# Kernel tuning notes

Measured on AMD Instinct MI355X. Metric: run time of the kernel, lower is better.

## Reference

```python
import jax, jax.numpy as jnp
import numpy as np

B, T, E, H, L, V = 16, 512, 512, 8, 4, 2048
HS = E // H  # head_size = n_embd // n_head
FF = 4 * E


def _ln(x, g, b):
    m = x.mean(-1, keepdims=True)
    v = ((x - m) ** 2).mean(-1, keepdims=True)
    return (x - m) * jax.lax.rsqrt(v + 1e-5) * g + b


def setup_inputs() -> dict:
    key = jax.random.key(0)
    ks = jax.random.split(key, 16)
    s = jnp.float32(0.02)
    return {
        "idx": jax.random.randint(ks[0], (B, T), 0, V),
        "tok_emb": jax.random.normal(ks[1], (V, E), jnp.float32) * s,
        "pos_emb": jax.random.normal(ks[2], (T, E), jnp.float32) * s,
        "Wq": jax.random.normal(ks[3], (L, E, E), jnp.float32) * s,
        "Wk": jax.random.normal(ks[4], (L, E, E), jnp.float32) * s,
        "Wv": jax.random.normal(ks[5], (L, E, E), jnp.float32) * s,
        "rel": jax.random.normal(ks[6], (L, 2 * T - 1, HS), jnp.float32) * s,
        "Wo": jax.random.normal(ks[7], (L, E, E), jnp.float32) * s,
        "bo": jnp.zeros((L, E), jnp.float32),
        "ln1_g": jnp.ones((L, E), jnp.float32),
        "ln1_b": jnp.zeros((L, E), jnp.float32),
        "W1": jax.random.normal(ks[8], (L, E, FF), jnp.float32) * s,
        "b1": jnp.zeros((L, FF), jnp.float32),
        "W2": jax.random.normal(ks[9], (L, FF, E), jnp.float32) * s,
        "b2": jnp.zeros((L, E), jnp.float32),
        "ln2_g": jnp.ones((L, E), jnp.float32),
        "ln2_b": jnp.zeros((L, E), jnp.float32),
        "lnf_g": jnp.ones((E,), jnp.float32),
        "lnf_b": jnp.zeros((E,), jnp.float32),
        "Wlm": jax.random.normal(ks[10], (E, V), jnp.float32) * s,
        "blm": jnp.zeros((V,), jnp.float32),
    }


def reference(idx, tok_emb, pos_emb, Wq, Wk, Wv, rel, Wo, bo, ln1_g, ln1_b,
              W1, b1, W2, b2, ln2_g, ln2_b, lnf_g, lnf_b, Wlm, blm):
    x = tok_emb[idx] + pos_emb[None, :T]  # (B,T,E)
    ri = jnp.arange(T)
    rel_idx = ri[:, None] - ri[None, :] + (T - 1)  # block_size == T
    causal = ri[:, None] >= ri[None, :]            # (T,T) lower-triangular
    scale = jnp.float32(1.0 / np.sqrt(HS))
    for l in range(L):
        h = _ln(x, ln1_g[l], ln1_b[l])
        # NOTE: torch code does .view(B, H, T, HS) on a (B, T, H*HS) tensor
        # (NOT a transpose) -- jnp.reshape matches row-major view semantics.
        q = (h @ Wq[l]).reshape(B, H, T, HS)
        k = (h @ Wk[l]).reshape(B, H, T, HS)
        v = (h @ Wv[l]).reshape(B, H, T, HS)
        re = rel[l][rel_idx]  # (T,T,HS)
        # rel scores: sum_d q[b,h,i,d]*re[i,j,d]; avoid the 5D intermediate
        scores = jnp.einsum('bhid,bhjd->bhij', q, k) * scale \
               + jnp.einsum('bhid,ijd->bhij', q, re)
        scores = jnp.where(causal, scores, -jnp.inf)
        att = jax.nn.softmax(scores, axis=-1)  # dropout disabled (eval)
        ctx = jnp.einsum('bhij,bhjd->bhid', att, v)
        ctx = jnp.swapaxes(ctx, 1, 2).reshape(B, T, H * HS)
        x = x + ctx @ Wo[l] + bo[l]
        h2 = _ln(x, ln2_g[l], ln2_b[l])
        x = x + jax.nn.relu(h2 @ W1[l] + b1[l]) @ W2[l] + b2[l]
    x = _ln(x, lnf_g, lnf_b)
    return x @ Wlm + blm  # logits (B,T,V)
```

## Files before the change

### kernel.cpp

```cpp
#include <hip/hip_runtime.h>
#include <hip/hip_bf16.h>
#include <stdint.h>

typedef __hip_bfloat16 bf16;
typedef __attribute__((ext_vector_type(8))) short bf16x8;
typedef __attribute__((ext_vector_type(8))) short short8;
typedef __attribute__((ext_vector_type(4))) float f32x4;

#define DEV __device__ __forceinline__

static constexpr int Bn = 16, Tn = 512, En = 512, Hn = 8, Ln = 4, Vn = 2048;
static constexpr int HSn = 64, FFn = 2048, Mn = Bn * Tn;
static constexpr int SQ = 1536;

DEV f32x4 mfma16(bf16x8 a, bf16x8 b, f32x4 c) {
  return __builtin_amdgcn_mfma_f32_16x16x32_bf16(a, b, c, 0, 0, 0);
}
DEV float b2f(bf16 x) { return __bfloat162float(x); }
DEV bf16 f2b(float x) { return __float2bfloat16(x); }
DEV short f2s(float x) { bf16 h = f2b(x); return reinterpret_cast<short&>(h); }

DEV void gload16(const void* g, void* l) {
  __builtin_amdgcn_global_load_lds(
      (const __attribute__((address_space(1))) void*)(uintptr_t)g,
      (__attribute__((address_space(3))) void*)(uint32_t)(uintptr_t)l, 16, 0, 0);
}

__global__ __launch_bounds__(256) void ktranspose(const float* __restrict__ in,
                                                  bf16* __restrict__ out, int R, int C,
                                                  long in_zs, long out_zs) {
  __shared__ float tile[32][33];
  int z = blockIdx.z;
  const float* inz = in + (size_t)z * in_zs;
  bf16* outz = out + (size_t)z * out_zs;
  int c0 = blockIdx.x * 32, r0 = blockIdx.y * 32;
  for (int k = 0; k < 32; k += 8)
    tile[threadIdx.y + k][threadIdx.x] =
        inz[(size_t)(r0 + threadIdx.y + k) * C + (c0 + threadIdx.x)];
  __syncthreads();
  for (int k = 0; k < 32; k += 8)
    outz[(size_t)(c0 + threadIdx.y + k) * R + (r0 + threadIdx.x)] =
        f2b(tile[threadIdx.x][threadIdx.y + k]);
}

__global__ __launch_bounds__(256) void kcast(const float* __restrict__ in,
                                             bf16* __restrict__ out, int n) {
  int i = blockIdx.x * 256 + threadIdx.x;
  if (i < n) out[i] = f2b(in[i]);
}

__global__ __launch_bounds__(256) void kembed(const int* __restrict__ idx,
                                              const float* __restrict__ tok,
                                              const float* __restrict__ pos,
                                              float* __restrict__ x) {
  int i = blockIdx.x * 256 + threadIdx.x;
  int e4 = (i & 127) * 4;
  int bt = i >> 7;
  int t = bt & (Tn - 1);
  f32x4 tv = *(const f32x4*)(tok + (size_t)idx[bt] * En + e4);
  f32x4 pv = *(const f32x4*)(pos + (size_t)t * En + e4);
  *(f32x4*)(x + (size_t)bt * En + e4) = tv + pv;
}

__global__ __launch_bounds__(256) void kln(const float* __restrict__ x,
                                           const float* __restrict__ g,
                                           const float* __restrict__ b,
                                           bf16* __restrict__ out) {
  int row = blockIdx.x * 4 + (threadIdx.x >> 6);
  int lane = threadIdx.x & 63;
  const float* xr = x + (size_t)row * En + lane * 8;
  f32x4 a0 = *(const f32x4*)xr;
  f32x4 a1 = *(const f32x4*)(xr + 4);
  float s = a0[0] + a0[1] + a0[2] + a0[3] + a1[0] + a1[1] + a1[2] + a1[3];
  for (int m = 1; m < 64; m <<= 1) s += __shfl_xor(s, m);
  float mean = s * (1.f / En);
  float s2 = 0.f;
  for (int j = 0; j < 4; j++) { float d0 = a0[j] - mean, d1 = a1[j] - mean; s2 += d0 * d0 + d1 * d1; }
  for (int m = 1; m < 64; m <<= 1) s2 += __shfl_xor(s2, m);
  float rstd = rsqrtf(s2 * (1.f / En) + 1e-5f);
  f32x4 g0 = *(const f32x4*)(g + lane * 8), g1 = *(const f32x4*)(g + lane * 8 + 4);
  f32x4 b0 = *(const f32x4*)(b + lane * 8), b1 = *(const f32x4*)(b + lane * 8 + 4);
  short8 ov;
  for (int j = 0; j < 4; j++) {
    ov[j] = f2s((a0[j] - mean) * rstd * g0[j] + b0[j]);
    ov[j + 4] = f2s((a1[j] - mean) * rstd * g1[j] + b1[j]);
  }
  *(short8*)(out + (size_t)row * En + lane * 8) = ov;
}

template <int BM, int BN, int TW, int DB, int SWZ, int NBIAS, int RELU, int MODE>
__global__ __launch_bounds__(TW) void kgemm(const bf16* __restrict__ A,
                                            const bf16* __restrict__ Bt,
                                            const float* __restrict__ bias,
                                            float* __restrict__ outf,
                                            bf16* __restrict__ outh, int Ndim, int K) {
  constexpr int NW = TW / 64;
  constexpr int WCN = NW / 2;
  constexpr int WM = BM / 2, WN = BN / WCN, MI = WM / 16, NI = WN / 16;
  constexpr int NB = DB ? 2 : 1;
  __shared__ bf16 As[NB][BM * 64];
  __shared__ bf16 Bs[NB][BN * 64];
  int t = threadIdx.x, lane = t & 63, w = t >> 6;
  int lr = lane & 15, lg = lane >> 4;
  int sx = lr & 7;
  int wr = w / WCN, wc = w % WCN;
  int bx, by;
  if (SWZ) {
    int id = blockIdx.x + gridDim.x * blockIdx.y;
    int xcd = id & 7, s = id >> 3;
    int gx = gridDim.x;
    by = xcd * 8 + s / gx;
    bx = s % gx;
  } else {
    bx = blockIdx.x; by = blockIdx.y;
  }
  int br = by * BM, bc = bx * BN;
  f32x4 acc[MI][NI] = {};
  int rl = lane >> 3, cb = (lane & 7) ^ rl;
  const bf16* Abase = A + (size_t)(br + w * (BM / NW) + rl) * K + cb * 8;
  const bf16* Bbase = Bt + (size_t)(bc + w * (BN / NW) + rl) * K + cb * 8;

  auto STAGE = [&](int buf, int kt) {
    for (int c = 0; c < BM / (8 * NW); c++)
      gload16(Abase + (size_t)(c * 8) * K + kt, &As[buf][(w * (BM / NW) + c * 8) * 64]);
    for (int c = 0; c < BN / (8 * NW); c++)
      gload16(Bbase + (size_t)(c * 8) * K + kt, &Bs[buf][(w * (BN / NW) + c * 8) * 64]);
  };
  auto COMPUTE = [&](int buf) {
    for (int kk = 0; kk < 2; kk++) {
      int gb = (kk * 4 + lg) ^ sx;
      bf16x8 af[MI], bfr[NI];
      for (int mi = 0; mi < MI; mi++)
        af[mi] = *(const bf16x8*)&As[buf][(wr * WM + mi * 16 + lr) * 64 + gb * 8];
      for (int ni = 0; ni < NI; ni++)
        bfr[ni] = *(const bf16x8*)&Bs[buf][(wc * WN + ni * 16 + lr) * 64 + gb * 8];
      for (int mi = 0; mi < MI; mi++)
        for (int ni = 0; ni < NI; ni++)
          acc[mi][ni] = mfma16(af[mi], bfr[ni], acc[mi][ni]);
    }
  };

  if (DB) {
    STAGE(0, 0);
    __syncthreads();
    int nt = K / 64;
    for (int t2 = 0; t2 < nt; t2++) {
      int cur = t2 & 1;
      if (t2 + 1 < nt) STAGE(cur ^ 1, (t2 + 1) * 64);
      COMPUTE(cur);
      __syncthreads();
    }
  } else {
    for (int kt = 0; kt < K; kt += 64) {
      __syncthreads();
      STAGE(0, kt);
      __syncthreads();
      COMPUTE(0);
    }
  }

  for (int mi = 0; mi < MI; mi++)
    for (int ni = 0; ni < NI; ni++)
      for (int r = 0; r < 4; r++) {
        int row = br + wr * WM + mi * 16 + lg * 4 + r;
        int col = bc + wc * WN + ni * 16 + lr;
        float val = acc[mi][ni][r];
        if (NBIAS) val += bias[col];
        if (RELU) val = fmaxf(val, 0.f);
        if (MODE == 1) outf[(size_t)row * Ndim + col] += val;
        else if (MODE == 2) outf[(size_t)row * Ndim + col] = val;
        else outh[(size_t)row * Ndim + col] = f2b(val);
      }
}

__global__ __launch_bounds__(256) void kattn(const bf16* __restrict__ qkv,
                                             const bf16* __restrict__ rel,
                                             bf16* __restrict__ ctx) {
  __shared__ bf16 Ks[128 * 64];
  __shared__ bf16 Vs[64 * 128];
  __shared__ bf16 Prel[4][16 * 81];
  __shared__ bf16 Ps[4][16 * 64];
  int pairp = blockIdx.x, bh = blockIdx.y;
  int b = bh >> 3, hh = bh & 7;
  int t = threadIdx.x, lane = t & 63, w = t >> 6;
  int lr = lane & 15, lg = lane >> 4;
  int sx = lr & 7;
  int rl8 = lane >> 3, cbk = (lane & 7) ^ rl8;
  const size_t headrow = (size_t)(b * Tn + hh * 64);
  bf16* prw = &Prel[w][0];
  bf16* psw = &Ps[w][0];
  int jp = t >> 3, db = (t & 7) * 8;

  for (int ph = 0; ph < 2; ph++) {
    int iblk = ph ? (7 - pairp) : pairp;
    int i0w = iblk * 64 + w * 16;
    bf16x8 aq[2];
    {
      int t2 = i0w + lr;
      const bf16* qp = qkv + (headrow + (t2 >> 3)) * SQ + (t2 & 7) * 64;
      aq[0] = *(const bf16x8*)(qp + lg * 8);
      aq[1] = *(const bf16x8*)(qp + 32 + lg * 8);
    }
    f32x4 o[4] = {};
    float m_run = -3e38f, l_run = 0.f;
    int ntiles = (iblk >> 1) + 1;

    for (int jt = 0; jt < ntiles; jt++) {
      int jbase = jt * 128;
      bf16x8 vv[4];
#pragma unroll
      for (int u = 0; u < 4; u++) {
        int j0 = jbase + jp * 4 + u;
        vv[u] = *(const bf16x8*)(qkv + (headrow + (j0 >> 3)) * SQ + (j0 & 7) * 64 + 1024 + db);
      }
      __syncthreads();
#pragma unroll
      for (int c = 0; c < 4; c++) {
        int row = w * 32 + c * 8 + rl8;
        const bf16* src = qkv + (headrow + ((jbase + row) >> 3)) * SQ +
                          (row & 7) * 64 + 512 + cbk * 8;
        gload16(src, &Ks[(w * 32 + c * 8) * 64]);
      }
#pragma unroll
      for (int pr = 0; pr < 2; pr++) {
        const short* pa = (const short*)&vv[pr * 2];
        const short* pb = (const short*)&vv[pr * 2 + 1];
        int j0 = jp * 4 + pr * 2;
        int jblk = j0 >> 3, jin = j0 & 7;
#pragma unroll
        for (int u = 0; u < 8; u++) {
          int d = db + u;
          int idx = d * 128 + ((jblk ^ (d & 7)) * 8) + jin;
          uint32_t pk = (uint32_t)(uint16_t)pa[u] | ((uint32_t)(uint16_t)pb[u] << 16);
          *(uint32_t*)((short*)Vs + idx) = pk;
        }
      }
      __syncthreads();
#pragma unroll
      for (int su = 0; su < 2; su++) {
        int jb = jbase + su * 64;
        if (jb > iblk * 64) break;
        bool diag = (jb == iblk * 64);
        int njmax = diag ? w : 3;
        int nmmin = diag ? 3 - w : 0;
        __builtin_amdgcn_s_setprio(1);
        f32x4 sqk[4] = {};
        for (int nj = 0; nj <= njmax; nj++) {
          int row = su * 64 + nj * 16 + lr;
          bf16x8 kb0 = *(const bf16x8*)&Ks[row * 64 + ((lg ^ sx) * 8)];
          bf16x8 kb1 = *(const bf16x8*)&Ks[row * 64 + (((4 + lg) ^ sx) * 8)];
          sqk[nj] = mfma16(kb0, aq[0], sqk[nj]);
          sqk[nj] = mfma16(kb1, aq[1], sqk[nj]);
        }
        int base = i0w - jb + 448;
        for (int nm = nmmin; nm < 5; nm++) {
          int mrow = base + nm * 16 + lr;
          if (mrow > 1022) mrow = 1022;
          const bf16* rp = rel + (size_t)mrow * 64;
          f32x4 sr = {};
          sr = mfma16(aq[0], *(const bf16x8*)(rp + lg * 8), sr);
          sr = mfma16(aq[1], *(const bf16x8*)(rp + 32 + lg * 8), sr);
          for (int r = 0; r < 4; r++)
            prw[(lg * 4 + r) * 81 + nm * 16 + lr] = f2b(sr[r]);
        }
        __builtin_amdgcn_s_setprio(0);
        float sv[4][4];
        for (int nj = 0; nj < 4; nj++)
          for (int r = 0; r < 4; r++) sv[nj][r] = -3e38f;
        float mloc = -3e38f;
        for (int nj = 0; nj <= njmax; nj++)
          for (int r = 0; r < 4; r++) {
            int jj = nj * 16 + lg * 4 + r;
            float val = sqk[nj][r] * 0.125f + b2f(prw[lr * 81 + (lr - jj + 63)]);
            if (jb + jj > i0w + lr) val = -3e38f;
            sv[nj][r] = val;
            mloc = fmaxf(mloc, val);
          }
        mloc = fmaxf(mloc, __shfl_xor(mloc, 16));
        mloc = fmaxf(mloc, __shfl_xor(mloc, 32));
        float mnew = fmaxf(m_run, mloc);
        float corr = __expf(m_run - mnew);
        m_run = mnew;
        float lsum = 0.f;
        for (int nj = 0; nj < 4; nj++)
          for (int r = 0; r < 4; r++) {
            float p = __expf(sv[nj][r] - mnew);
            lsum += p;
            psw[lr * 64 + (((nj * 2 + (lg >> 1)) ^ sx) * 8) + (lg & 1) * 4 + r] = f2b(p);
          }
        lsum += __shfl_xor(lsum, 16);
        lsum += __shfl_xor(lsum, 32);
        l_run = l_run * corr + lsum;
        for (int r = 0; r < 4; r++) {
          float c = __shfl(corr, lg * 4 + r);
          for (int nd = 0; nd < 4; nd++) o[nd][r] *= c;
        }
        __builtin_amdgcn_s_setprio(1);
        bf16x8 ap0 = *(const bf16x8*)&psw[lr * 64 + ((lg ^ sx) * 8)];
        bf16x8 ap1 = *(const bf16x8*)&psw[lr * 64 + (((4 + lg) ^ sx) * 8)];
        for (int nd = 0; nd < 4; nd++) {
          int d = nd * 16 + lr;
          bf16x8 vb0 = *(const bf16x8*)&Vs[d * 128 + ((su * 8 + (lg ^ sx)) * 8)];
          bf16x8 vb1 = *(const bf16x8*)&Vs[d * 128 + ((su * 8 + ((4 + lg) ^ sx)) * 8)];
          o[nd] = mfma16(ap0, vb0, o[nd]);
          o[nd] = mfma16(ap1, vb1, o[nd]);
        }
        __builtin_amdgcn_s_setprio(0);
      }
    }
    for (int r = 0; r < 4; r++) {
      float linv = 1.f / __shfl(l_run, lg * 4 + r);
      int row = i0w + lg * 4 + r;
      for (int nd = 0; nd < 4; nd++)
        ctx[((size_t)b * Tn + row) * En + hh * 64 + nd * 16 + lr] = f2b(o[nd][r] * linv);
    }
  }
}

extern "C" void kernel_launch(void* const* d_in, const int* in_sizes, int n_in,
                              void* d_out, int out_size, void* d_ws, size_t ws_size,
                              hipStream_t stream) {
  (void)in_sizes; (void)n_in; (void)out_size; (void)ws_size;
  const int* idx = (const int*)d_in[0];
  const float* tok = (const float*)d_in[1];
  const float* pos = (const float*)d_in[2];
  const float* Wq = (const float*)d_in[3];
  const float* Wk = (const float*)d_in[4];
  const float* Wv = (const float*)d_in[5];
  const float* rel = (const float*)d_in[6];
  const float* Wo = (const float*)d_in[7];
  const float* bo = (const float*)d_in[8];
  const float* ln1_g = (const float*)d_in[9];
  const float* ln1_b = (const float*)d_in[10];
  const float* W1 = (const float*)d_in[11];
  const float* b1 = (const float*)d_in[12];
  const float* W2 = (const float*)d_in[13];
  const float* b2 = (const float*)d_in[14];
  const float* ln2_g = (const float*)d_in[15];
  const float* ln2_b = (const float*)d_in[16];
  const float* lnf_g = (const float*)d_in[17];
  const float* lnf_b = (const float*)d_in[18];
  const float* Wlm = (const float*)d_in[19];
  const float* blm = (const float*)d_in[20];

  char* ws = (char*)d_ws;
  float* x = (float*)(ws + 0);
  bf16* h = (bf16*)(ws + 16777216);
  bf16* qkv = (bf16*)(ws + 25165824);
  bf16* ctx = (bf16*)(ws + 50331648);
  bf16* ffn1 = qkv;
  bf16* wqkvT = (bf16*)(ws + 58720256);
  bf16* woT = wqkvT + (size_t)Ln * SQ * En;
  bf16* w1T = woT + (size_t)Ln * En * En;
  bf16* w2T = w1T + (size_t)Ln * En * FFn;
  bf16* wlmT = w2T + (size_t)Ln * FFn * En;
  bf16* relc = wlmT + (size_t)En * Vn;
  float* outf = (float*)d_out;

  dim3 tb(32, 8);
  ktranspose<<<dim3(16, 16, Ln), tb, 0, stream>>>(Wq, wqkvT, En, En, (long)En * En, (long)SQ * En);
  ktranspose<<<dim3(16, 16, Ln), tb, 0, stream>>>(Wk, wqkvT + 512 * 512, En, En, (long)En * En, (long)SQ * En);
  ktranspose<<<dim3(16, 16, Ln), tb, 0, stream>>>(Wv, wqkvT + 2 * 512 * 512, En, En, (long)En * En, (long)SQ * En);
  ktranspose<<<dim3(16, 16, Ln), tb, 0, stream>>>(Wo, woT, En, En, (long)En * En, (long)En * En);
  ktranspose<<<dim3(64, 16, Ln), tb, 0, stream>>>(W1, w1T, En, FFn, (long)En * FFn, (long)En * FFn);
  ktranspose<<<dim3(16, 64, Ln), tb, 0, stream>>>(W2, w2T, FFn, En, (long)FFn * En, (long)FFn * En);
  ktranspose<<<dim3(64, 16, 1), tb, 0, stream>>>(Wlm, wlmT, En, Vn, 0, 0);
  kcast<<<(Ln * (2 * Tn - 1) * HSn + 255) / 256, 256, 0, stream>>>(
      rel, relc, Ln * (2 * Tn - 1) * HSn);

  kembed<<<(Mn * En / 4) / 256, 256, 0, stream>>>(idx, tok, pos, x);

  for (int l = 0; l < Ln; l++) {
    kln<<<Mn / 4, 256, 0, stream>>>(x, ln1_g + (size_t)l * En, ln1_b + (size_t)l * En, h);
    kgemm<128, 128, 512, 1, 1, 0, 0, 0><<<dim3(12, 64), 512, 0, stream>>>(
        h, wqkvT + (size_t)l * SQ * En, nullptr, nullptr, qkv, SQ, En);
    kattn<<<dim3(4, 128), 256, 0, stream>>>(
        qkv, relc + (size_t)l * (2 * Tn - 1) * HSn, ctx);
    kgemm<128, 128, 512, 1, 1, 1, 0, 1><<<dim3(4, 64), 512, 0, stream>>>(
        ctx, woT + (size_t)l * En * En, bo + (size_t)l * En, x, nullptr, En, En);
    kln<<<Mn / 4, 256, 0, stream>>>(x, ln2_g + (size_t)l * En, ln2_b + (size_t)l * En, h);
    kgemm<128, 128, 512, 1, 1, 1, 1, 0><<<dim3(16, 64), 512, 0, stream>>>(
        h, w1T + (size_t)l * En * FFn, b1 + (size_t)l * FFn, nullptr, ffn1, FFn, En);
    kgemm<128, 128, 512, 1, 1, 1, 0, 1><<<dim3(4, 64), 512, 0, stream>>>(
        ffn1, w2T + (size_t)l * FFn * En, b2 + (size_t)l * En, x, nullptr, En, FFn);
  }
  kln<<<Mn / 4, 256, 0, stream>>>(x, lnf_g, lnf_b, h);
  kgemm<128, 128, 512, 1, 1, 1, 0, 2><<<dim3(16, 64), 512, 0, stream>>>(
      h, wlmT, blm, outf, nullptr, Vn, En);
}
```

Before: 668.9 us.

## Share K/V tiles across paired query blocks in attention; retune GEMM threads

The attention kernel previously handled its two paired query blocks (pairp and 7-pairp) one after the other, reloading K and V tiles for each. It now walks the key tiles once and updates both query blocks' online-softmax states from each shared tile, cutting global loads and barriers. This keeps two sets of accumulators live, which raises register pressure and may lower occupancy. Separately, the QKV, FFN1 and LM-head GEMMs switch to a 256-thread configuration with a different template flag.

```diff
diff --git a/kernel.cpp b/kernel.cpp
--- a/kernel.cpp
+++ b/kernel.cpp
@@ -191,129 +191,140 @@
   bf16* psw = &Ps[w][0];
   int jp = t >> 3, db = (t & 7) * 8;
 
-  for (int ph = 0; ph < 2; ph++) {
-    int iblk = ph ? (7 - pairp) : pairp;
-    int i0w = iblk * 64 + w * 16;
-    bf16x8 aq[2];
-    {
-      int t2 = i0w + lr;
-      const bf16* qp = qkv + (headrow + (t2 >> 3)) * SQ + (t2 & 7) * 64;
-      aq[0] = *(const bf16x8*)(qp + lg * 8);
-      aq[1] = *(const bf16x8*)(qp + 32 + lg * 8);
-    }
-    f32x4 o[4] = {};
-    float m_run = -3e38f, l_run = 0.f;
-    int ntiles = (iblk >> 1) + 1;
-
-    for (int jt = 0; jt < ntiles; jt++) {
-      int jbase = jt * 128;
-      bf16x8 vv[4];
+  int ia = pairp, ib = 7 - pairp;
+  int i0a = ia * 64 + w * 16, i0b = ib * 64 + w * 16;
+  bf16x8 aqa[2], aqb[2];
+  {
+    int t2 = i0a + lr;
+    const bf16* qp = qkv + (headrow + (t2 >> 3)) * SQ + (t2 & 7) * 64;
+    aqa[0] = *(const bf16x8*)(qp + lg * 8);
+    aqa[1] = *(const bf16x8*)(qp + 32 + lg * 8);
+    t2 = i0b + lr;
+    qp = qkv + (headrow + (t2 >> 3)) * SQ + (t2 & 7) * 64;
+    aqb[0] = *(const bf16x8*)(qp + lg * 8);
+    aqb[1] = *(const bf16x8*)(qp + 32 + lg * 8);
+  }
+  f32x4 oa[4] = {}, ob[4] = {};
+  float m_a = -3e38f, l_a = 0.f, m_b = -3e38f, l_b = 0.f;
+  int ntiles = (ib >> 1) + 1;
+
+  auto SUBTILE = [&](const bf16x8* aq, f32x4* o, float& m_run, float& l_run,
+                     int i0w, int jb, bool diag, int su) {
+    int njmax = diag ? w : 3;
+    int nmmin = diag ? 3 - w : 0;
+    __builtin_amdgcn_s_setprio(1);
+    f32x4 sqk[4] = {};
+    for (int nj = 0; nj <= njmax; nj++) {
+      int row = su * 64 + nj * 16 + lr;
+      bf16x8 kb0 = *(const bf16x8*)&Ks[row * 64 + ((lg ^ sx) * 8)];
+      bf16x8 kb1 = *(const bf16x8*)&Ks[row * 64 + (((4 + lg) ^ sx) * 8)];
+      sqk[nj] = mfma16(kb0, aq[0], sqk[nj]);
+      sqk[nj] = mfma16(kb1, aq[1], sqk[nj]);
+    }
+    int base = i0w - jb + 448;
+    for (int nm = nmmin; nm < 5; nm++) {
+      int mrow = base + nm * 16 + lr;
+      if (mrow > 1022) mrow = 1022;
+      const bf16* rp = rel + (size_t)mrow * 64;
+      f32x4 sr = {};
+      sr = mfma16(aq[0], *(const bf16x8*)(rp + lg * 8), sr);
+      sr = mfma16(aq[1], *(const bf16x8*)(rp + 32 + lg * 8), sr);
+      for (int r = 0; r < 4; r++)
+        prw[(lg * 4 + r) * 81 + nm * 16 + lr] = f2b(sr[r]);
+    }
+    __builtin_amdgcn_s_setprio(0);
+    float sv[4][4];
+    for (int nj = 0; nj < 4; nj++)
+      for (int r = 0; r < 4; r++) sv[nj][r] = -3e38f;
+    float mloc = -3e38f;
+    for (int nj = 0; nj <= njmax; nj++)
+      for (int r = 0; r < 4; r++) {
+        int jj = nj * 16 + lg * 4 + r;
+        float val = sqk[nj][r] * 0.125f + b2f(prw[lr * 81 + (lr - jj + 63)]);
+        if (jb + jj > i0w + lr) val = -3e38f;
+        sv[nj][r] = val;
+        mloc = fmaxf(mloc, val);
+      }
+    mloc = fmaxf(mloc, __shfl_xor(mloc, 16));
+    mloc = fmaxf(mloc, __shfl_xor(mloc, 32));
+    float mnew = fmaxf(m_run, mloc);
+    float corr = __expf(m_run - mnew);
+    m_run = mnew;
+    float lsum = 0.f;
+    for (int nj = 0; nj < 4; nj++)
+      for (int r = 0; r < 4; r++) {
+        float p = __expf(sv[nj][r] - mnew);
+        lsum += p;
+        psw[lr * 64 + (((nj * 2 + (lg >> 1)) ^ sx) * 8) + (lg & 1) * 4 + r] = f2b(p);
+      }
+    lsum += __shfl_xor(lsum, 16);
+    lsum += __shfl_xor(lsum, 32);
+    l_run = l_run * corr + lsum;
+    for (int r = 0; r < 4; r++) {
+      float c = __shfl(corr, lg * 4 + r);
+      for (int nd = 0; nd < 4; nd++) o[nd][r] *= c;
+    }
+    __builtin_amdgcn_s_setprio(1);
+    bf16x8 ap0 = *(const bf16x8*)&psw[lr * 64 + ((lg ^ sx) * 8)];
+    bf16x8 ap1 = *(const bf16x8*)&psw[lr * 64 + (((4 + lg) ^ sx) * 8)];
+    for (int nd = 0; nd < 4; nd++) {
+      int d = nd * 16 + lr;
+      bf16x8 vb0 = *(const bf16x8*)&Vs[d * 128 + ((su * 8 + (lg ^ sx)) * 8)];
+      bf16x8 vb1 = *(const bf16x8*)&Vs[d * 128 + ((su * 8 + ((4 + lg) ^ sx)) * 8)];
+      o[nd] = mfma16(ap0, vb0, o[nd]);
+      o[nd] = mfma16(ap1, vb1, o[nd]);
+    }
+    __builtin_amdgcn_s_setprio(0);
+  };
+
+  for (int jt = 0; jt < ntiles; jt++) {
+    int jbase = jt * 128;
+    bf16x8 vv[4];
 #pragma unroll
-      for (int u = 0; u < 4; u++) {
-        int j0 = jbase + jp * 4 + u;
-        vv[u] = *(const bf16x8*)(qkv + (headrow + (j0 >> 3)) * SQ + (j0 & 7) * 64 + 1024 + db);
+    for (int u = 0; u < 4; u++) {
+      int j0 = jbase + jp * 4 + u;
+      vv[u] = *(const bf16x8*)(qkv + (headrow + (j0 >> 3)) * SQ + (j0 & 7) * 64 + 1024 + db);
+    }
+    __syncthreads();
+#pragma unroll
+    for (int c = 0; c < 4; c++) {
+      int row = w * 32 + c * 8 + rl8;
+      const bf16* src = qkv + (headrow + ((jbase + row) >> 3)) * SQ +
+                        (row & 7) * 64 + 512 + cbk * 8;
+      gload16(src, &Ks[(w * 32 + c * 8) * 64]);
+    }
+#pragma unroll
+    for (int pr = 0; pr < 2; pr++) {
+      const short* pa = (const short*)&vv[pr * 2];
+      const short* pb = (const short*)&vv[pr * 2 + 1];
+      int j0 = jp * 4 + pr * 2;
+      int jblk = j0 >> 3, jin = j0 & 7;
+#pragma unroll
+      for (int u = 0; u < 8; u++) {
+        int d = db + u;
+        int idx = d * 128 + ((jblk ^ (d & 7)) * 8) + jin;
+        uint32_t pk = (uint32_t)(uint16_t)pa[u] | ((uint32_t)(uint16_t)pb[u] << 16);
+        *(uint32_t*)((short*)Vs + idx) = pk;
       }
-      __syncthreads();
+    }
+    __syncthreads();
 #pragma unroll
-      for (int c = 0; c < 4; c++) {
-        int row = w * 32 + c * 8 + rl8;
-        const bf16* src = qkv + (headrow + ((jbase + row) >> 3)) * SQ +
-                          (row & 7) * 64 + 512 + cbk * 8;
-        gload16(src, &Ks[(w * 32 + c * 8) * 64]);
-      }
-#pragma unroll
-      for (int pr = 0; pr < 2; pr++) {
-        const short* pa = (const short*)&vv[pr * 2];
-        const short* pb = (const short*)&vv[pr * 2 + 1];
-        int j0 = jp * 4 + pr * 2;
-        int jblk = j0 >> 3, jin = j0 & 7;
-#pragma unroll
-        for (int u = 0; u < 8; u++) {
-          int d = db + u;
-          int idx = d * 128 + ((jblk ^ (d & 7)) * 8) + jin;
-          uint32_t pk = (uint32_t)(uint16_t)pa[u] | ((uint32_t)(uint16_t)pb[u] << 16);
-          *(uint32_t*)((short*)Vs + idx) = pk;
-        }
-      }
-      __syncthreads();
-#pragma unroll
-      for (int su = 0; su < 2; su++) {
-        int jb = jbase + su * 64;
-        if (jb > iblk * 64) break;
-        bool diag = (jb == iblk * 64);
-        int njmax = diag ? w : 3;
-        int nmmin = diag ? 3 - w : 0;
-        __builtin_amdgcn_s_setprio(1);
-        f32x4 sqk[4] = {};
-        for (int nj = 0; nj <= njmax; nj++) {
-          int row = su * 64 + nj * 16 + lr;
-          bf16x8 kb0 = *(const bf16x8*)&Ks[row * 64 + ((lg ^ sx) * 8)];
-          bf16x8 kb1 = *(const bf16x8*)&Ks[row * 64 + (((4 + lg) ^ sx) * 8)];
-          sqk[nj] = mfma16(kb0, aq[0], sqk[nj]);
-          sqk[nj] = mfma16(kb1, aq[1], sqk[nj]);
-        }
-        int base = i0w - jb + 448;
-        for (int nm = nmmin; nm < 5; nm++) {
-          int mrow = base + nm * 16 + lr;
-          if (mrow > 1022) mrow = 1022;
-          const bf16* rp = rel + (size_t)mrow * 64;
-          f32x4 sr = {};
-          sr = mfma16(aq[0], *(const bf16x8*)(rp + lg * 8), sr);
-          sr = mfma16(aq[1], *(const bf16x8*)(rp + 32 + lg * 8), sr);
-          for (int r = 0; r < 4; r++)
-            prw[(lg * 4 + r) * 81 + nm * 16 + lr] = f2b(sr[r]);
-        }
-        __builtin_amdgcn_s_setprio(0);
-        float sv[4][4];
-        for (int nj = 0; nj < 4; nj++)
-          for (int r = 0; r < 4; r++) sv[nj][r] = -3e38f;
-        float mloc = -3e38f;
-        for (int nj = 0; nj <= njmax; nj++)
-          for (int r = 0; r < 4; r++) {
-            int jj = nj * 16 + lg * 4 + r;
-            float val = sqk[nj][r] * 0.125f + b2f(prw[lr * 81 + (lr - jj + 63)]);
-            if (jb + jj > i0w + lr) val = -3e38f;
-            sv[nj][r] = val;
-            mloc = fmaxf(mloc, val);
-          }
-        mloc = fmaxf(mloc, __shfl_xor(mloc, 16));
-        mloc = fmaxf(mloc, __shfl_xor(mloc, 32));
-        float mnew = fmaxf(m_run, mloc);
-        float corr = __expf(m_run - mnew);
-        m_run = mnew;
-        float lsum = 0.f;
-        for (int nj = 0; nj < 4; nj++)
-          for (int r = 0; r < 4; r++) {
-            float p = __expf(sv[nj][r] - mnew);
-            lsum += p;
-            psw[lr * 64 + (((nj * 2 + (lg >> 1)) ^ sx) * 8) + (lg & 1) * 4 + r] = f2b(p);
-          }
-        lsum += __shfl_xor(lsum, 16);
-        lsum += __shfl_xor(lsum, 32);
-        l_run = l_run * corr + lsum;
-        for (int r = 0; r < 4; r++) {
-          float c = __shfl(corr, lg * 4 + r);
-          for (int nd = 0; nd < 4; nd++) o[nd][r] *= c;
-        }
-        __builtin_amdgcn_s_setprio(1);
-        bf16x8 ap0 = *(const bf16x8*)&psw[lr * 64 + ((lg ^ sx) * 8)];
-        bf16x8 ap1 = *(const bf16x8*)&psw[lr * 64 + (((4 + lg) ^ sx) * 8)];
-        for (int nd = 0; nd < 4; nd++) {
-          int d = nd * 16 + lr;
-          bf16x8 vb0 = *(const bf16x8*)&Vs[d * 128 + ((su * 8 + (lg ^ sx)) * 8)];
-          bf16x8 vb1 = *(const bf16x8*)&Vs[d * 128 + ((su * 8 + ((4 + lg) ^ sx)) * 8)];
-          o[nd] = mfma16(ap0, vb0, o[nd]);
-          o[nd] = mfma16(ap1, vb1, o[nd]);
-        }
-        __builtin_amdgcn_s_setprio(0);
-      }
-    }
-    for (int r = 0; r < 4; r++) {
-      float linv = 1.f / __shfl(l_run, lg * 4 + r);
-      int row = i0w + lg * 4 + r;
-      for (int nd = 0; nd < 4; nd++)
-        ctx[((size_t)b * Tn + row) * En + hh * 64 + nd * 16 + lr] = f2b(o[nd][r] * linv);
-    }
+    for (int su = 0; su < 2; su++) {
+      int jb = jbase + su * 64;
+      if (jb > ib * 64) break;
+      SUBTILE(aqb, ob, m_b, l_b, i0b, jb, jb == ib * 64, su);
+      if (jb <= ia * 64) SUBTILE(aqa, oa, m_a, l_a, i0a, jb, jb == ia * 64, su);
+    }
+  }
+  for (int r = 0; r < 4; r++) {
+    float linv = 1.f / __shfl(l_a, lg * 4 + r);
+    int row = i0a + lg * 4 + r;
+    for (int nd = 0; nd < 4; nd++)
+      ctx[((size_t)b * Tn + row) * En + hh * 64 + nd * 16 + lr] = f2b(oa[nd][r] * linv);
+    linv = 1.f / __shfl(l_b, lg * 4 + r);
+    row = i0b + lg * 4 + r;
+    for (int nd = 0; nd < 4; nd++)
+      ctx[((size_t)b * Tn + row) * En + hh * 64 + nd * 16 + lr] = f2b(ob[nd][r] * linv);
   }
 }
 
@@ -372,19 +383,19 @@
 
   for (int l = 0; l < Ln; l++) {
     kln<<<Mn / 4, 256, 0, stream>>>(x, ln1_g + (size_t)l * En, ln1_b + (size_t)l * En, h);
-    kgemm<128, 128, 512, 1, 1, 0, 0, 0><<<dim3(12, 64), 512, 0, stream>>>(
+    kgemm<128, 128, 256, 0, 1, 0, 0, 0><<<dim3(12, 64), 256, 0, stream>>>(
         h, wqkvT + (size_t)l * SQ * En, nullptr, nullptr, qkv, SQ, En);
     kattn<<<dim3(4, 128), 256, 0, stream>>>(
         qkv, relc + (size_t)l * (2 * Tn - 1) * HSn, ctx);
     kgemm<128, 128, 512, 1, 1, 1, 0, 1><<<dim3(4, 64), 512, 0, stream>>>(
         ctx, woT + (size_t)l * En * En, bo + (size_t)l * En, x, nullptr, En, En);
     kln<<<Mn / 4, 256, 0, stream>>>(x, ln2_g + (size_t)l * En, ln2_b + (size_t)l * En, h);
-    kgemm<128, 128, 512, 1, 1, 1, 1, 0><<<dim3(16, 64), 512, 0, stream>>>(
+    kgemm<128, 128, 256, 0, 1, 1, 1, 0><<<dim3(16, 64), 256, 0, stream>>>(
         h, w1T + (size_t)l * En * FFn, b1 + (size_t)l * FFn, nullptr, ffn1, FFn, En);
     kgemm<128, 128, 512, 1, 1, 1, 0, 1><<<dim3(4, 64), 512, 0, stream>>>(
         ffn1, w2T + (size_t)l * FFn * En, b2 + (size_t)l * En, x, nullptr, En, FFn);
   }
   kln<<<Mn / 4, 256, 0, stream>>>(x, lnf_g, lnf_b, h);
-  kgemm<128, 128, 512, 1, 1, 1, 0, 2><<<dim3(16, 64), 512, 0, stream>>>(
+  kgemm<128, 128, 256, 0, 1, 1, 0, 2><<<dim3(16, 64), 256, 0, stream>>>(
       h, wlmT, blm, outf, nullptr, Vn, En);
 }
```

After: 656.9 us. Within noise of the previous version (-1.8%).

## Run both causal query blocks concurrently in 512-thread attention blocks; retune GEMM threads

Applied to the files above, without the earlier changes.

The attention kernel now launches 8 waves per block. Each group of four waves owns one of the paired query blocks (iblk and 7-iblk), so the two phases run concurrently instead of in sequence, and the K/V tiles are loaded once into shared memory and shared by both groups. Waves whose block ends earlier skip the later subtiles but still join the barriers. Separately, the QKV, FFN1 and LM-head GEMMs switch to a 256-thread configuration with a different template flag, which trades per-block parallelism for possibly higher occupancy.

```diff
diff --git a/kernel.cpp b/kernel.cpp
--- a/kernel.cpp
+++ b/kernel.cpp
@@ -173,16 +173,17 @@
       }
 }
 
-__global__ __launch_bounds__(256) void kattn(const bf16* __restrict__ qkv,
+__global__ __launch_bounds__(512) void kattn(const bf16* __restrict__ qkv,
                                              const bf16* __restrict__ rel,
                                              bf16* __restrict__ ctx) {
   __shared__ bf16 Ks[128 * 64];
   __shared__ bf16 Vs[64 * 128];
-  __shared__ bf16 Prel[4][16 * 81];
-  __shared__ bf16 Ps[4][16 * 64];
+  __shared__ bf16 Prel[8][16 * 81];
+  __shared__ bf16 Ps[8][16 * 64];
   int pairp = blockIdx.x, bh = blockIdx.y;
   int b = bh >> 3, hh = bh & 7;
   int t = threadIdx.x, lane = t & 63, w = t >> 6;
+  int wl = w & 3, wg = w >> 2;
   int lr = lane & 15, lg = lane >> 4;
   int sx = lr & 7;
   int rl8 = lane >> 3, cbk = (lane & 7) ^ rl8;
@@ -191,129 +192,131 @@
   bf16* psw = &Ps[w][0];
   int jp = t >> 3, db = (t & 7) * 8;
 
-  for (int ph = 0; ph < 2; ph++) {
-    int iblk = ph ? (7 - pairp) : pairp;
-    int i0w = iblk * 64 + w * 16;
-    bf16x8 aq[2];
+  int ia = pairp, ib = 7 - pairp;
+  int myblk = wg ? ia : ib;
+  int mylast = myblk * 64;
+  int i0w = myblk * 64 + wl * 16;
+  bf16x8 aq[2];
+  {
+    int t2 = i0w + lr;
+    const bf16* qp = qkv + (headrow + (t2 >> 3)) * SQ + (t2 & 7) * 64;
+    aq[0] = *(const bf16x8*)(qp + lg * 8);
+    aq[1] = *(const bf16x8*)(qp + 32 + lg * 8);
+  }
+  f32x4 o[4] = {};
+  float m_run = -3e38f, l_run = 0.f;
+  int ntiles = (ib >> 1) + 1;
+
+  auto SUBTILE = [&](int jb, bool diag, int su) {
+    int njmax = diag ? wl : 3;
+    int nmmin = diag ? 3 - wl : 0;
+    __builtin_amdgcn_s_setprio(1);
+    f32x4 sqk[4] = {};
+    for (int nj = 0; nj <= njmax; nj++) {
+      int row = su * 64 + nj * 16 + lr;
+      bf16x8 kb0 = *(const bf16x8*)&Ks[row * 64 + ((lg ^ sx) * 8)];
+      bf16x8 kb1 = *(const bf16x8*)&Ks[row * 64 + (((4 + lg) ^ sx) * 8)];
+      sqk[nj] = mfma16(kb0, aq[0], sqk[nj]);
+      sqk[nj] = mfma16(kb1, aq[1], sqk[nj]);
+    }
+    int base = i0w - jb + 448;
+    for (int nm = nmmin; nm < 5; nm++) {
+      int mrow = base + nm * 16 + lr;
+      if (mrow > 1022) mrow = 1022;
+      const bf16* rp = rel + (size_t)mrow * 64;
+      f32x4 sr = {};
+      sr = mfma16(aq[0], *(const bf16x8*)(rp + lg * 8), sr);
+      sr = mfma16(aq[1], *(const bf16x8*)(rp + 32 + lg * 8), sr);
+      for (int r = 0; r < 4; r++)
+        prw[(lg * 4 + r) * 81 + nm * 16 + lr] = f2b(sr[r]);
+    }
+    __builtin_amdgcn_s_setprio(0);
+    float sv[4][4];
+    for (int nj = 0; nj < 4; nj++)
+      for (int r = 0; r < 4; r++) sv[nj][r] = -3e38f;
+    float mloc = -3e38f;
+    for (int nj = 0; nj <= njmax; nj++)
+      for (int r = 0; r < 4; r++) {
+        int jj = nj * 16 + lg * 4 + r;
+        float val = sqk[nj][r] * 0.125f + b2f(prw[lr * 81 + (lr - jj + 63)]);
+        if (jb + jj > i0w + lr) val = -3e38f;
+        sv[nj][r] = val;
+        mloc = fmaxf(mloc, val);
+      }
+    mloc = fmaxf(mloc, __shfl_xor(mloc, 16));
+    mloc = fmaxf(mloc, __shfl_xor(mloc, 32));
+    float mnew = fmaxf(m_run, mloc);
+    float corr = __expf(m_run - mnew);
+    m_run = mnew;
+    float lsum = 0.f;
+    for (int nj = 0; nj < 4; nj++)
+      for (int r = 0; r < 4; r++) {
+        float p = __expf(sv[nj][r] - mnew);
+        lsum += p;
+        psw[lr * 64 + (((nj * 2 + (lg >> 1)) ^ sx) * 8) + (lg & 1) * 4 + r] = f2b(p);
+      }
+    lsum += __shfl_xor(lsum, 16);
+    lsum += __shfl_xor(lsum, 32);
+    l_run = l_run * corr + lsum;
+    for (int r = 0; r < 4; r++) {
+      float c = __shfl(corr, lg * 4 + r);
+      for (int nd = 0; nd < 4; nd++) o[nd][r] *= c;
+    }
+    __builtin_amdgcn_s_setprio(1);
+    bf16x8 ap0 = *(const bf16x8*)&psw[lr * 64 + ((lg ^ sx) * 8)];
+    bf16x8 ap1 = *(const bf16x8*)&psw[lr * 64 + (((4 + lg) ^ sx) * 8)];
+    for (int nd = 0; nd < 4; nd++) {
+      int d = nd * 16 + lr;
+      bf16x8 vb0 = *(const bf16x8*)&Vs[d * 128 + ((su * 8 + (lg ^ sx)) * 8)];
+      bf16x8 vb1 = *(const bf16x8*)&Vs[d * 128 + ((su * 8 + ((4 + lg) ^ sx)) * 8)];
+      o[nd] = mfma16(ap0, vb0, o[nd]);
+      o[nd] = mfma16(ap1, vb1, o[nd]);
+    }
+    __builtin_amdgcn_s_setprio(0);
+  };
+
+  for (int jt = 0; jt < ntiles; jt++) {
+    int jbase = jt * 128;
+    bf16x8 vv[2];
+#pragma unroll
+    for (int u = 0; u < 2; u++) {
+      int j0 = jbase + jp * 2 + u;
+      vv[u] = *(const bf16x8*)(qkv + (headrow + (j0 >> 3)) * SQ + (j0 & 7) * 64 + 1024 + db);
+    }
+    __syncthreads();
+#pragma unroll
+    for (int c = 0; c < 2; c++) {
+      int row = w * 16 + c * 8 + rl8;
+      const bf16* src = qkv + (headrow + ((jbase + row) >> 3)) * SQ +
+                        (row & 7) * 64 + 512 + cbk * 8;
+      gload16(src, &Ks[(w * 16 + c * 8) * 64]);
+    }
     {
-      int t2 = i0w + lr;
-      const bf16* qp = qkv + (headrow + (t2 >> 3)) * SQ + (t2 & 7) * 64;
-      aq[0] = *(const bf16x8*)(qp + lg * 8);
-      aq[1] = *(const bf16x8*)(qp + 32 + lg * 8);
-    }
-    f32x4 o[4] = {};
-    float m_run = -3e38f, l_run = 0.f;
-    int ntiles = (iblk >> 1) + 1;
-
-    for (int jt = 0; jt < ntiles; jt++) {
-      int jbase = jt * 128;
-      bf16x8 vv[4];
+      const short* pa = (const short*)&vv[0];
+      const short* pb = (const short*)&vv[1];
+      int j0 = jp * 2;
+      int jblk = j0 >> 3, jin = j0 & 7;
 #pragma unroll
-      for (int u = 0; u < 4; u++) {
-        int j0 = jbase + jp * 4 + u;
-        vv[u] = *(const bf16x8*)(qkv + (headrow + (j0 >> 3)) * SQ + (j0 & 7) * 64 + 1024 + db);
+      for (int u = 0; u < 8; u++) {
+        int d = db + u;
+        int idx = d * 128 + ((jblk ^ (d & 7)) * 8) + jin;
+        uint32_t pk = (uint32_t)(uint16_t)pa[u] | ((uint32_t)(uint16_t)pb[u] << 16);
+        *(uint32_t*)((short*)Vs + idx) = pk;
       }
-      __syncthreads();
+    }
+    __syncthreads();
 #pragma unroll
-      for (int c = 0; c < 4; c++) {
-        int row = w * 32 + c * 8 + rl8;
-        const bf16* src = qkv + (headrow + ((jbase + row) >> 3)) * SQ +
-                          (row & 7) * 64 + 512 + cbk * 8;
-        gload16(src, &Ks[(w * 32 + c * 8) * 64]);
-      }
-#pragma unroll
-      for (int pr = 0; pr < 2; pr++) {
-        const short* pa = (const short*)&vv[pr * 2];
-        const short* pb = (const short*)&vv[pr * 2 + 1];
-        int j0 = jp * 4 + pr * 2;
-        int jblk = j0 >> 3, jin = j0 & 7;
-#pragma unroll
-        for (int u = 0; u < 8; u++) {
-          int d = db + u;
-          int idx = d * 128 + ((jblk ^ (d & 7)) * 8) + jin;
-          uint32_t pk = (uint32_t)(uint16_t)pa[u] | ((uint32_t)(uint16_t)pb[u] << 16);
-          *(uint32_t*)((short*)Vs + idx) = pk;
-        }
-      }
-      __syncthreads();
-#pragma unroll
-      for (int su = 0; su < 2; su++) {
-        int jb = jbase + su * 64;
-        if (jb > iblk * 64) break;
-        bool diag = (jb == iblk * 64);
-        int njmax = diag ? w : 3;
-        int nmmin = diag ? 3 - w : 0;
-        __builtin_amdgcn_s_setprio(1);
-        f32x4 sqk[4] = {};
-        for (int nj = 0; nj <= njmax; nj++) {
-          int row = su * 64 + nj * 16 + lr;
-          bf16x8 kb0 = *(const bf16x8*)&Ks[row * 64 + ((lg ^ sx) * 8)];
-          bf16x8 kb1 = *(const bf16x8*)&Ks[row * 64 + (((4 + lg) ^ sx) * 8)];
-          sqk[nj] = mfma16(kb0, aq[0], sqk[nj]);
-          sqk[nj] = mfma16(kb1, aq[1], sqk[nj]);
-        }
-        int base = i0w - jb + 448;
-        for (int nm = nmmin; nm < 5; nm++) {
-          int mrow = base + nm * 16 + lr;
-          if (mrow > 1022) mrow = 1022;
-          const bf16* rp = rel + (size_t)mrow * 64;
-          f32x4 sr = {};
-          sr = mfma16(aq[0], *(const bf16x8*)(rp + lg * 8), sr);
-          sr = mfma16(aq[1], *(const bf16x8*)(rp + 32 + lg * 8), sr);
-          for (int r = 0; r < 4; r++)
-            prw[(lg * 4 + r) * 81 + nm * 16 + lr] = f2b(sr[r]);
-        }
-        __builtin_amdgcn_s_setprio(0);
-        float sv[4][4];
-        for (int nj = 0; nj < 4; nj++)
-          for (int r = 0; r < 4; r++) sv[nj][r] = -3e38f;
-        float mloc = -3e38f;
-        for (int nj = 0; nj <= njmax; nj++)
-          for (int r = 0; r < 4; r++) {
-            int jj = nj * 16 + lg * 4 + r;
-            float val = sqk[nj][r] * 0.125f + b2f(prw[lr * 81 + (lr - jj + 63)]);
-            if (jb + jj > i0w + lr) val = -3e38f;
-            sv[nj][r] = val;
-            mloc = fmaxf(mloc, val);
-          }
-        mloc = fmaxf(mloc, __shfl_xor(mloc, 16));
-        mloc = fmaxf(mloc, __shfl_xor(mloc, 32));
-        float mnew = fmaxf(m_run, mloc);
-        float corr = __expf(m_run - mnew);
-        m_run = mnew;
-        float lsum = 0.f;
-        for (int nj = 0; nj < 4; nj++)
-          for (int r = 0; r < 4; r++) {
-            float p = __expf(sv[nj][r] - mnew);
-            lsum += p;
-            psw[lr * 64 + (((nj * 2 + (lg >> 1)) ^ sx) * 8) + (lg & 1) * 4 + r] = f2b(p);
-          }
-        lsum += __shfl_xor(lsum, 16);
-        lsum += __shfl_xor(lsum, 32);
-        l_run = l_run * corr + lsum;
-        for (int r = 0; r < 4; r++) {
-          float c = __shfl(corr, lg * 4 + r);
-          for (int nd = 0; nd < 4; nd++) o[nd][r] *= c;
-        }
-        __builtin_amdgcn_s_setprio(1);
-        bf16x8 ap0 = *(const bf16x8*)&psw[lr * 64 + ((lg ^ sx) * 8)];
-        bf16x8 ap1 = *(const bf16x8*)&psw[lr * 64 + (((4 + lg) ^ sx) * 8)];
-        for (int nd = 0; nd < 4; nd++) {
-          int d = nd * 16 + lr;
-          bf16x8 vb0 = *(const bf16x8*)&Vs[d * 128 + ((su * 8 + (lg ^ sx)) * 8)];
-          bf16x8 vb1 = *(const bf16x8*)&Vs[d * 128 + ((su * 8 + ((4 + lg) ^ sx)) * 8)];
-          o[nd] = mfma16(ap0, vb0, o[nd]);
-          o[nd] = mfma16(ap1, vb1, o[nd]);
-        }
-        __builtin_amdgcn_s_setprio(0);
-      }
-    }
-    for (int r = 0; r < 4; r++) {
-      float linv = 1.f / __shfl(l_run, lg * 4 + r);
-      int row = i0w + lg * 4 + r;
-      for (int nd = 0; nd < 4; nd++)
-        ctx[((size_t)b * Tn + row) * En + hh * 64 + nd * 16 + lr] = f2b(o[nd][r] * linv);
-    }
+    for (int su = 0; su < 2; su++) {
+      int jb = jbase + su * 64;
+      if (jb > ib * 64) break;
+      if (jb <= mylast) SUBTILE(jb, jb == mylast, su);
+    }
+  }
+  for (int r = 0; r < 4; r++) {
+    float linv = 1.f / __shfl(l_run, lg * 4 + r);
+    int row = i0w + lg * 4 + r;
+    for (int nd = 0; nd < 4; nd++)
+      ctx[((size_t)b * Tn + row) * En + hh * 64 + nd * 16 + lr] = f2b(o[nd][r] * linv);
   }
 }
 
@@ -372,19 +375,19 @@
 
   for (int l = 0; l < Ln; l++) {
     kln<<<Mn / 4, 256, 0, stream>>>(x, ln1_g + (size_t)l * En, ln1_b + (size_t)l * En, h);
-    kgemm<128, 128, 512, 1, 1, 0, 0, 0><<<dim3(12, 64), 512, 0, stream>>>(
+    kgemm<128, 128, 256, 0, 1, 0, 0, 0><<<dim3(12, 64), 256, 0, stream>>>(
         h, wqkvT + (size_t)l * SQ * En, nullptr, nullptr, qkv, SQ, En);
-    kattn<<<dim3(4, 128), 256, 0, stream>>>(
+    kattn<<<dim3(4, 128), 512, 0, stream>>>(
         qkv, relc + (size_t)l * (2 * Tn - 1) * HSn, ctx);
     kgemm<128, 128, 512, 1, 1, 1, 0, 1><<<dim3(4, 64), 512, 0, stream>>>(
         ctx, woT + (size_t)l * En * En, bo + (size_t)l * En, x, nullptr, En, En);
     kln<<<Mn / 4, 256, 0, stream>>>(x, ln2_g + (size_t)l * En, ln2_b + (size_t)l * En, h);
-    kgemm<128, 128, 512, 1, 1, 1, 1, 0><<<dim3(16, 64), 512, 0, stream>>>(
+    kgemm<128, 128, 256, 0, 1, 1, 1, 0><<<dim3(16, 64), 256, 0, stream>>>(
         h, w1T + (size_t)l * En * FFn, b1 + (size_t)l * FFn, nullptr, ffn1, FFn, En);
     kgemm<128, 128, 512, 1, 1, 1, 0, 1><<<dim3(4, 64), 512, 0, stream>>>(
         ffn1, w2T + (size_t)l * FFn * En, b2 + (size_t)l * En, x, nullptr, En, FFn);
   }
   kln<<<Mn / 4, 256, 0, stream>>>(x, lnf_g, lnf_b, h);
-  kgemm<128, 128, 512, 1, 1, 1, 0, 2><<<dim3(16, 64), 512, 0, stream>>>(
+  kgemm<128, 128, 256, 0, 1, 1, 0, 2><<<dim3(16, 64), 256, 0, stream>>>(
       h, wlmT, blm, outf, nullptr, Vn, En);
 }
```

New measurement: 645.8 us. 1.04x faster.
